# Kernel tuning notes

Hardware: AMD Instinct MI355X
Metric: run time of the kernel (lower is better)

## Reference

```python
import jax, jax.numpy as jnp
import numpy as np

CTX = 1024   # context_window
D = 512      # emb_dim
B = 8        # batch


def make_rotary_matrix(ctx, d):
    """Dense block-diagonal RoPE rotation matrices R: [ctx, d, d]."""
    pos = jnp.arange(ctx, dtype=jnp.float32)[:, None]          # [ctx, 1]
    i = jnp.arange(d // 2, dtype=jnp.float32)                  # [d/2]
    theta = pos / (10000.0 ** (2.0 * i / d))                   # [ctx, d/2]
    cos, sin = jnp.cos(theta), jnp.sin(theta)
    idx = jnp.arange(d // 2)
    R = jnp.zeros((ctx, d, d), jnp.float32)
    R = R.at[:, 2 * idx, 2 * idx].set(cos)
    R = R.at[:, 2 * idx, 2 * idx + 1].set(-sin)
    R = R.at[:, 2 * idx + 1, 2 * idx].set(sin)
    R = R.at[:, 2 * idx + 1, 2 * idx + 1].set(cos)
    return R


def setup_inputs() -> dict:
    key = jax.random.key(0)
    ks = jax.random.split(key, 8)
    s = 1.0 / np.sqrt(D)
    inp = {
        "x": jax.random.normal(ks[0], (B, CTX, D), jnp.float32),
        "w_q": jax.random.uniform(ks[1], (D, D), jnp.float32, -s, s),
        "b_q": jax.random.uniform(ks[2], (D,), jnp.float32, -s, s),
        "w_k": jax.random.uniform(ks[3], (D, D), jnp.float32, -s, s),
        "b_k": jax.random.uniform(ks[4], (D,), jnp.float32, -s, s),
        "w_v": jax.random.uniform(ks[5], (D, D), jnp.float32, -s, s),
        "b_v": jax.random.uniform(ks[6], (D,), jnp.float32, -s, s),
        "R": make_rotary_matrix(CTX, D),
        "kv_cache": 0,  # bool flag; does not affect output
    }
    return inp


def reference(x, w_q, b_q, w_k, b_k, w_v, b_v, R, kv_cache):
    B_, C, Dm = x.shape
    q = x @ w_q.T + b_q                      # [B, C, D]
    k = x @ w_k.T + b_k
    v = x @ w_v.T + b_v
    Rc = R[:C]                               # [C, D, D]
    # torch.bmm(q.transpose(0,1), R.transpose(1,2)).transpose(0,1)
    # out[b,c,e] = sum_d q[b,c,d] * R[c,e,d]
    q_rot = jnp.einsum("bcd,ced->bce", q, Rc)
    k_rot = jnp.einsum("bcd,ced->bce", k, Rc)
    # causal SDPA (eval mode: dropout omitted)
    scale = 1.0 / jnp.sqrt(jnp.asarray(Dm, jnp.float32))
    scores = jnp.einsum("bqe,bke->bqk", q_rot, k_rot) * scale   # [B, C, C]
    causal = jnp.tril(jnp.ones((C, C), bool))
    scores = jnp.where(causal, scores, jnp.finfo(scores.dtype).min)
    attn = jax.nn.softmax(scores, axis=-1)
    return jnp.einsum("bqk,bkd->bqd", attn, v)
```

## Files before the change

### kernel.cpp

```cpp
#include <hip/hip_runtime.h>

#define BATCH 8
#define CTXN  1024
#define DMODEL 512

using short8  = __attribute__((ext_vector_type(8))) short;
using f32x16  = __attribute__((ext_vector_type(16))) float;

typedef const void __attribute__((address_space(1)))* as1_cvp;
typedef void __attribute__((address_space(3)))* as3_vp;

__device__ __forceinline__ unsigned short f2bf(float f) {
  unsigned int u = __float_as_uint(f);
  u += 0x7fffu + ((u >> 16) & 1u);
  return (unsigned short)(u >> 16);
}
__device__ __forceinline__ float bf2f(unsigned short u) {
  return __uint_as_float((unsigned int)u << 16);
}

#define X4  1048576
#define W4  65536
#define CAST_BLOCKS 4864
__global__ __launch_bounds__(256) void prep_all(const float* __restrict__ x,
                                                const float* __restrict__ wq,
                                                const float* __restrict__ wk,
                                                const float* __restrict__ wv,
                                                unsigned short* __restrict__ xb,
                                                unsigned short* __restrict__ wb,
                                                float2* __restrict__ tab) {
  if (blockIdx.x < CAST_BLOCKS) {
    int gid = blockIdx.x * 256 + threadIdx.x;
    const float4* src; ushort4* dst;
    if (gid < X4)                { src = (const float4*)x  + gid;              dst = (ushort4*)xb + gid; }
    else if (gid < X4 + W4)      { int o = gid - X4;        src = (const float4*)wq + o; dst = (ushort4*)wb + o; }
    else if (gid < X4 + 2 * W4)  { int o = gid - X4 - W4;   src = (const float4*)wk + o; dst = (ushort4*)(wb + 262144) + o; }
    else                         { int o = gid - X4 - 2*W4; src = (const float4*)wv + o; dst = (ushort4*)(wb + 524288) + o; }
    float4 f = *src;
    ushort4 u;
    u.x = f2bf(f.x); u.y = f2bf(f.y); u.z = f2bf(f.z); u.w = f2bf(f.w);
    *dst = u;
  } else {
    int c = blockIdx.x - CAST_BLOCKS;
    int i = threadIdx.x;
    float freq = exp2f((float)i * (-13.287712379549449f / 256.0f));
    float th = (float)c * freq;
    float sn, cs;
    sincosf(th, &sn, &cs);
    tab[c * 256 + i] = make_float2(cs, sn);
  }
}


__device__ __forceinline__ void issue_tile(const unsigned short* __restrict__ gA, int ldA,
                                           const unsigned short* __restrict__ gB, int ldB,
                                           unsigned short* sA, unsigned short* sB,
                                           int slot, int tid) {
  unsigned short* dA = sA + (slot << 13);
  unsigned short* dB = sB + (slot << 13);
#pragma unroll
  for (int c = 0; c < 4; ++c) {
    int li  = (c << 8) + tid;
    int row = li >> 3;
    int ch  = (li & 7) ^ (row & 7);
    __builtin_amdgcn_global_load_lds((as1_cvp)(gA + (size_t)row * ldA + (ch << 3)),
                                     (as3_vp)(dA + (li << 3)), 16, 0, 0);
  }
#pragma unroll
  for (int c = 0; c < 4; ++c) {
    int li  = (c << 8) + tid;
    int row = li >> 3;
    int ch  = (li & 7) ^ (row & 7);
    __builtin_amdgcn_global_load_lds((as1_cvp)(gB + (size_t)row * ldB + (ch << 3)),
                                     (as3_vp)(dB + (li << 3)), 16, 0, 0);
  }
}

__device__ __forceinline__ void gemm_pipe(const unsigned short* __restrict__ gA, int ldA,
                                          const unsigned short* __restrict__ gB, int ldB,
                                          int nt, unsigned short* sA, unsigned short* sB,
                                          int tid, f32x16 acc[2][2]) {
  const int l = tid & 63, w = tid >> 6, wr = w >> 1, wc = w & 1;
  const int cl = l & 31, hi = l >> 5;
  int aoff[2][4], boff[2][4];
#pragma unroll
  for (int m = 0; m < 2; ++m) {
    int ra = wr * 64 + m * 32 + cl;
    int rb = wc * 64 + m * 32 + cl;
#pragma unroll
    for (int ks = 0; ks < 4; ++ks) {
      int kc = ks * 2 + hi;
      aoff[m][ks] = ra * 64 + ((kc ^ (ra & 7)) << 3);
      boff[m][ks] = rb * 64 + ((kc ^ (rb & 7)) << 3);
    }
  }
  issue_tile(gA, ldA, gB, ldB, sA, sB, 0, tid);
  issue_tile(gA + 64, ldA, gB + 64, ldB, sA, sB, 1, tid);
  asm volatile("s_waitcnt vmcnt(8)" ::: "memory");
  __builtin_amdgcn_s_barrier();
  __builtin_amdgcn_sched_barrier(0);

  for (int t = 0; t < nt; ++t) {
    const unsigned short* sAb = sA + ((t & 1) << 13);
    const unsigned short* sBb = sB + ((t & 1) << 13);
    short8 af[2][4], bfv[2][4];
    af[0][0] = *(const short8*)(sAb + aoff[0][0]);
    af[1][0] = *(const short8*)(sAb + aoff[1][0]);
    bfv[0][0] = *(const short8*)(sBb + boff[0][0]);
    bfv[1][0] = *(const short8*)(sBb + boff[1][0]);
#pragma unroll
    for (int ks = 0; ks < 3; ++ks) {
      af[0][ks + 1] = *(const short8*)(sAb + aoff[0][ks + 1]);
      af[1][ks + 1] = *(const short8*)(sAb + aoff[1][ks + 1]);
      bfv[0][ks + 1] = *(const short8*)(sBb + boff[0][ks + 1]);
      bfv[1][ks + 1] = *(const short8*)(sBb + boff[1][ks + 1]);
      asm volatile("s_waitcnt lgkmcnt(4)" ::: "memory");
      __builtin_amdgcn_sched_barrier(0);
      __builtin_amdgcn_s_setprio(1);
#pragma unroll
      for (int m = 0; m < 2; ++m)
#pragma unroll
        for (int n = 0; n < 2; ++n)
          acc[m][n] = __builtin_amdgcn_mfma_f32_32x32x16_bf16(af[m][ks], bfv[n][ks], acc[m][n], 0, 0, 0);
      __builtin_amdgcn_s_setprio(0);
    }
    asm volatile("s_waitcnt lgkmcnt(0)" ::: "memory");
    __builtin_amdgcn_sched_barrier(0);
    __builtin_amdgcn_s_barrier();
    if (t + 2 < nt) {
      issue_tile(gA + (size_t)(t + 2) * 64, ldA, gB + (size_t)(t + 2) * 64, ldB, sA, sB, t & 1, tid);
      asm volatile("s_waitcnt vmcnt(8)" ::: "memory");
    } else {
      asm volatile("s_waitcnt vmcnt(0)" ::: "memory");
    }
    __builtin_amdgcn_sched_barrier(0);
    __builtin_amdgcn_s_setprio(1);
#pragma unroll
    for (int m = 0; m < 2; ++m)
#pragma unroll
      for (int n = 0; n < 2; ++n)
        acc[m][n] = __builtin_amdgcn_mfma_f32_32x32x16_bf16(af[m][3], bfv[n][3], acc[m][n], 0, 0, 0);
    __builtin_amdgcn_s_setprio(0);
    __builtin_amdgcn_s_barrier();
    __builtin_amdgcn_sched_barrier(0);
  }
}


__global__ __launch_bounds__(256) void qkv_kernel(const unsigned short* __restrict__ xb,
                                                  const unsigned short* __restrict__ wb,
                                                  const float* __restrict__ bq,
                                                  const float* __restrict__ bk,
                                                  const float* __restrict__ bv,
                                                  const float2* __restrict__ tab,
                                                  unsigned short* __restrict__ qrot,
                                                  unsigned short* __restrict__ krot,
                                                  unsigned short* __restrict__ vt) {
  __shared__ __align__(16) unsigned short sA[2 * 8192];
  __shared__ __align__(16) unsigned short sB[2 * 8192];
  int t = threadIdx.x, w = t >> 6, l = t & 63, wr = w >> 1, wc = w & 1;
  int cl = l & 31, hi = l >> 5;
  int m0 = blockIdx.x * 128, n0 = blockIdx.y * 128;
  f32x16 acc[2][2] = {};
  gemm_pipe(xb + (size_t)m0 * 512, 512, wb + (size_t)n0 * 512, 512, 8, sA, sB, t, acc);

  int sec = n0 >> 9;
  const float* bias = (sec == 0) ? bq : (sec == 1) ? bk : bv;
  unsigned short* qk_dst = (sec == 0) ? qrot : krot;
#pragma unroll
  for (int n = 0; n < 2; ++n) {
    int eg = n0 + wc * 64 + n * 32 + cl;
    int e  = eg & 511;
    float bsv = bias[e];
    if (sec < 2) {
      int i2 = e >> 1;
#pragma unroll
      for (int m = 0; m < 2; ++m) {
        int rowb = m0 + wr * 64 + m * 32 + 4 * hi;
#pragma unroll
        for (int r = 0; r < 16; ++r) {
          int mg = rowb + (r & 3) + 8 * (r >> 2);
          int cpos = mg & (CTXN - 1);
          float val  = acc[m][n][r] + bsv;
          float part = __shfl_xor(val, 1);
          float2 cs  = tab[cpos * 256 + i2];
          float o = (e & 1) ? fmaf(part, cs.y, val * cs.x)
                            : fmaf(-part, cs.y, val * cs.x);
          qk_dst[(size_t)mg * 512 + e] = f2bf(o);
        }
      }
    } else {
#pragma unroll
      for (int m = 0; m < 2; ++m) {
        int rowb0 = m0 + wr * 64 + m * 32 + 4 * hi;
#pragma unroll
        for (int q = 0; q < 4; ++q) {
          int rowb = rowb0 + 8 * q;
          int bidx = rowb >> 10;
          int cpos = rowb & (CTXN - 1);
          ushort4 pk;
          pk.x = f2bf(acc[m][n][q * 4 + 0] + bsv);
          pk.y = f2bf(acc[m][n][q * 4 + 1] + bsv);
          pk.z = f2bf(acc[m][n][q * 4 + 2] + bsv);
          pk.w = f2bf(acc[m][n][q * 4 + 3] + bsv);
          *(ushort4*)(vt + ((size_t)bidx * 512 + e) * 1024 + cpos) = pk;
        }
      }
    }
  }
}

__device__ const unsigned char TRI_IT[36] = {0,1,1,2,2,2,3,3,3,3,4,4,4,4,4,5,5,5,5,5,5,
                                             6,6,6,6,6,6,6,7,7,7,7,7,7,7,7};
__device__ const unsigned char TRI_JT[36] = {0,0,1,0,1,2,0,1,2,3,0,1,2,3,4,0,1,2,3,4,5,
                                             0,1,2,3,4,5,6,0,1,2,3,4,5,6,7};

__global__ __launch_bounds__(256) void scores_kernel(const unsigned short* __restrict__ qr,
                                                     const unsigned short* __restrict__ kr,
                                                     unsigned short* __restrict__ S) {
  int it = TRI_IT[blockIdx.x], jt = TRI_JT[blockIdx.x], b = blockIdx.y;
  __shared__ __align__(16) unsigned short sA[2 * 8192];
  __shared__ __align__(16) unsigned short sB[2 * 8192];
  int t = threadIdx.x, w = t >> 6, l = t & 63, wr = w >> 1, wc = w & 1;
  int cl = l & 31, hi = l >> 5;
  const unsigned short* A  = qr + ((size_t)b << 19) + (size_t)it * 128 * 512;
  const unsigned short* Bp = kr + ((size_t)b << 19) + (size_t)jt * 128 * 512;
  f32x16 acc[2][2] = {};
  gemm_pipe(A, 512, Bp, 512, 8, sA, sB, t, acc);

  const float scale = 0.04419417382415922f;
  unsigned short* Sb = S + ((size_t)b << 20);
#pragma unroll
  for (int m = 0; m < 2; ++m) {
    int iqb = it * 128 + wr * 64 + m * 32 + 4 * hi;
#pragma unroll
    for (int n = 0; n < 2; ++n) {
      int j = jt * 128 + wc * 64 + n * 32 + cl;
#pragma unroll
      for (int r = 0; r < 16; ++r)
        Sb[(size_t)(iqb + (r & 3) + 8 * (r >> 2)) * 1024 + j] = f2bf(acc[m][n][r] * scale);
    }
  }
}

__global__ __launch_bounds__(256) void softmax_kernel(const unsigned short* __restrict__ S,
                                                      unsigned short* __restrict__ P) {
  int w = threadIdx.x >> 6, l = threadIdx.x & 63;
  int i = blockIdx.x * 4 + w;
  int b = blockIdx.y;
  const unsigned short* row = S + ((size_t)b << 20) + (size_t)i * 1024;
  unsigned short* prow = P + ((size_t)b << 20) + (size_t)i * 1024;
  int len  = i + 1;
  int jmax = ((i >> 7) + 1) << 7;
  float v[16];
  float mx = -3.4e38f;
#pragma unroll
  for (int c = 0; c < 2; ++c) {
    short8 raw = *(const short8*)(row + c * 512 + l * 8);
#pragma unroll
    for (int jj = 0; jj < 8; ++jj) {
      int j = c * 512 + l * 8 + jj;
      float f = bf2f((unsigned short)raw[jj]);
      v[c * 8 + jj] = (j < len) ? f : -3.4e38f;
      mx = fmaxf(mx, v[c * 8 + jj]);
    }
  }
#pragma unroll
  for (int o = 32; o > 0; o >>= 1) mx = fmaxf(mx, __shfl_xor(mx, o));
  float sm = 0.0f;
#pragma unroll
  for (int p = 0; p < 16; ++p) {
    int j = (p >> 3) * 512 + l * 8 + (p & 7);
    v[p] = (j < len) ? __expf(v[p] - mx) : 0.0f;
    sm += v[p];
  }
#pragma unroll
  for (int o = 32; o > 0; o >>= 1) sm += __shfl_xor(sm, o);
  float inv = 1.0f / sm;
#pragma unroll
  for (int c = 0; c < 2; ++c) {
    int jbase = c * 512 + l * 8;
    if (jbase < jmax) {
      short8 outv;
#pragma unroll
      for (int jj = 0; jj < 8; ++jj) outv[jj] = (short)f2bf(v[c * 8 + jj] * inv);
      *(short8*)(prow + jbase) = outv;
    }
  }
}

__global__ __launch_bounds__(256) void pv_kernel(const unsigned short* __restrict__ P,
                                                 const unsigned short* __restrict__ vt,
                                                 float* __restrict__ out) {
  int it = blockIdx.x, nt2 = blockIdx.y, b = blockIdx.z;
  __shared__ __align__(16) unsigned short sA[2 * 8192];
  __shared__ __align__(16) unsigned short sB[2 * 8192];
  int t = threadIdx.x, w = t >> 6, l = t & 63, wr = w >> 1, wc = w & 1;
  int cl = l & 31, hi = l >> 5;
  const unsigned short* A  = P  + ((size_t)b << 20) + (size_t)it * 128 * 1024;
  const unsigned short* Bp = vt + ((size_t)b << 19) + (size_t)nt2 * 128 * 1024;
  int nt = (it + 1) * 2;
  f32x16 acc[2][2] = {};
  gemm_pipe(A, 1024, Bp, 1024, nt, sA, sB, t, acc);

  float* ob = out + ((size_t)b << 19);
#pragma unroll
  for (int m = 0; m < 2; ++m) {
    int iqb = it * 128 + wr * 64 + m * 32 + 4 * hi;
#pragma unroll
    for (int n = 0; n < 2; ++n) {
      int d = nt2 * 128 + wc * 64 + n * 32 + cl;
#pragma unroll
      for (int r = 0; r < 16; ++r)
        ob[(size_t)(iqb + (r & 3) + 8 * (r >> 2)) * 512 + d] = acc[m][n][r];
    }
  }
}

extern "C" void kernel_launch(void* const* d_in, const int* in_sizes, int n_in,
                              void* d_out, int out_size, void* d_ws, size_t ws_size,
                              hipStream_t stream) {
  const float* x  = (const float*)d_in[0];
  const float* wq = (const float*)d_in[1];
  const float* bq = (const float*)d_in[2];
  const float* wk = (const float*)d_in[3];
  const float* bk = (const float*)d_in[4];
  const float* wv = (const float*)d_in[5];
  const float* bv = (const float*)d_in[6];
  float* out = (float*)d_out;

  char* ws = (char*)d_ws;
  float2*         tab  = (float2*)(ws);
  unsigned short* xb   = (unsigned short*)(ws + (2ull  << 20));
  unsigned short* wb   = (unsigned short*)(ws + (10ull << 20));
  unsigned short* qrot = (unsigned short*)(ws + (12ull << 20));
  unsigned short* krot = (unsigned short*)(ws + (20ull << 20));
  unsigned short* vt   = (unsigned short*)(ws + (28ull << 20));
  unsigned short* S    = (unsigned short*)(ws + (36ull << 20));
  unsigned short* P    = (unsigned short*)(ws + (52ull << 20));

  prep_all<<<dim3(CAST_BLOCKS + CTXN), dim3(256), 0, stream>>>(x, wq, wk, wv, xb, wb, tab);
  qkv_kernel<<<dim3(64, 12), dim3(256), 0, stream>>>(xb, wb, bq, bk, bv, tab, qrot, krot, vt);
  scores_kernel<<<dim3(36, BATCH), dim3(256), 0, stream>>>(qrot, krot, S);
  softmax_kernel<<<dim3(256, BATCH), dim3(256), 0, stream>>>(S, P);
  pv_kernel<<<dim3(8, 4, BATCH), dim3(256), 0, stream>>>(P, vt, out);
}
```

Before: 77.79 us.

## Use 8 waves per block with 2x4 wave grid in shared GEMM pipeline

Each 128x128 GEMM tile is now computed by 512 threads (8 waves in a 2x4 layout) instead of 256 (4 waves in 2x2), so each wave owns a 64x32 sub-tile with two accumulators. Loads per thread into LDS are halved and the waitcnt thresholds are adjusted to match. The aim is more waves per CU to hide latency and a lower register footprint per wave. In exchange, each wave gets less B-fragment reuse and barrier cost rises with more waves per block.

```diff
diff --git a/kernel.cpp b/kernel.cpp
--- a/kernel.cpp
+++ b/kernel.cpp
@@ -59,16 +59,16 @@
   unsigned short* dA = sA + (slot << 13);
   unsigned short* dB = sB + (slot << 13);
 #pragma unroll
-  for (int c = 0; c < 4; ++c) {
-    int li  = (c << 8) + tid;
+  for (int c = 0; c < 2; ++c) {
+    int li  = (c << 9) + tid;
     int row = li >> 3;
     int ch  = (li & 7) ^ (row & 7);
     __builtin_amdgcn_global_load_lds((as1_cvp)(gA + (size_t)row * ldA + (ch << 3)),
                                      (as3_vp)(dA + (li << 3)), 16, 0, 0);
   }
 #pragma unroll
-  for (int c = 0; c < 4; ++c) {
-    int li  = (c << 8) + tid;
+  for (int c = 0; c < 2; ++c) {
+    int li  = (c << 9) + tid;
     int row = li >> 3;
     int ch  = (li & 7) ^ (row & 7);
     __builtin_amdgcn_global_load_lds((as1_cvp)(gB + (size_t)row * ldB + (ch << 3)),
@@ -79,49 +79,50 @@
 __device__ __forceinline__ void gemm_pipe(const unsigned short* __restrict__ gA, int ldA,
                                           const unsigned short* __restrict__ gB, int ldB,
                                           int nt, unsigned short* sA, unsigned short* sB,
-                                          int tid, f32x16 acc[2][2]) {
-  const int l = tid & 63, w = tid >> 6, wr = w >> 1, wc = w & 1;
+                                          int tid, f32x16 acc[2]) {
+  const int l = tid & 63, w = tid >> 6, wr = w >> 2, wc = w & 3;
   const int cl = l & 31, hi = l >> 5;
-  int aoff[2][4], boff[2][4];
+  int aoff[2][4], boff[4];
 #pragma unroll
   for (int m = 0; m < 2; ++m) {
     int ra = wr * 64 + m * 32 + cl;
-    int rb = wc * 64 + m * 32 + cl;
 #pragma unroll
     for (int ks = 0; ks < 4; ++ks) {
       int kc = ks * 2 + hi;
       aoff[m][ks] = ra * 64 + ((kc ^ (ra & 7)) << 3);
-      boff[m][ks] = rb * 64 + ((kc ^ (rb & 7)) << 3);
+    }
+  }
+  {
+    int rb = wc * 32 + cl;
+#pragma unroll
+    for (int ks = 0; ks < 4; ++ks) {
+      int kc = ks * 2 + hi;
+      boff[ks] = rb * 64 + ((kc ^ (rb & 7)) << 3);
     }
   }
   issue_tile(gA, ldA, gB, ldB, sA, sB, 0, tid);
   issue_tile(gA + 64, ldA, gB + 64, ldB, sA, sB, 1, tid);
-  asm volatile("s_waitcnt vmcnt(8)" ::: "memory");
+  asm volatile("s_waitcnt vmcnt(4)" ::: "memory");
   __builtin_amdgcn_s_barrier();
   __builtin_amdgcn_sched_barrier(0);
 
   for (int t = 0; t < nt; ++t) {
     const unsigned short* sAb = sA + ((t & 1) << 13);
     const unsigned short* sBb = sB + ((t & 1) << 13);
-    short8 af[2][4], bfv[2][4];
+    short8 af[2][4], bfv[4];
     af[0][0] = *(const short8*)(sAb + aoff[0][0]);
     af[1][0] = *(const short8*)(sAb + aoff[1][0]);
-    bfv[0][0] = *(const short8*)(sBb + boff[0][0]);
-    bfv[1][0] = *(const short8*)(sBb + boff[1][0]);
+    bfv[0]   = *(const short8*)(sBb + boff[0]);
 #pragma unroll
     for (int ks = 0; ks < 3; ++ks) {
       af[0][ks + 1] = *(const short8*)(sAb + aoff[0][ks + 1]);
       af[1][ks + 1] = *(const short8*)(sAb + aoff[1][ks + 1]);
-      bfv[0][ks + 1] = *(const short8*)(sBb + boff[0][ks + 1]);
-      bfv[1][ks + 1] = *(const short8*)(sBb + boff[1][ks + 1]);
-      asm volatile("s_waitcnt lgkmcnt(4)" ::: "memory");
+      bfv[ks + 1]   = *(const short8*)(sBb + boff[ks + 1]);
+      asm volatile("s_waitcnt lgkmcnt(3)" ::: "memory");
       __builtin_amdgcn_sched_barrier(0);
       __builtin_amdgcn_s_setprio(1);
-#pragma unroll
-      for (int m = 0; m < 2; ++m)
-#pragma unroll
-        for (int n = 0; n < 2; ++n)
-          acc[m][n] = __builtin_amdgcn_mfma_f32_32x32x16_bf16(af[m][ks], bfv[n][ks], acc[m][n], 0, 0, 0);
+      acc[0] = __builtin_amdgcn_mfma_f32_32x32x16_bf16(af[0][ks], bfv[ks], acc[0], 0, 0, 0);
+      acc[1] = __builtin_amdgcn_mfma_f32_32x32x16_bf16(af[1][ks], bfv[ks], acc[1], 0, 0, 0);
       __builtin_amdgcn_s_setprio(0);
     }
     asm volatile("s_waitcnt lgkmcnt(0)" ::: "memory");
@@ -129,17 +130,14 @@
     __builtin_amdgcn_s_barrier();
     if (t + 2 < nt) {
       issue_tile(gA + (size_t)(t + 2) * 64, ldA, gB + (size_t)(t + 2) * 64, ldB, sA, sB, t & 1, tid);
-      asm volatile("s_waitcnt vmcnt(8)" ::: "memory");
+      asm volatile("s_waitcnt vmcnt(4)" ::: "memory");
     } else {
       asm volatile("s_waitcnt vmcnt(0)" ::: "memory");
     }
     __builtin_amdgcn_sched_barrier(0);
     __builtin_amdgcn_s_setprio(1);
-#pragma unroll
-    for (int m = 0; m < 2; ++m)
-#pragma unroll
-      for (int n = 0; n < 2; ++n)
-        acc[m][n] = __builtin_amdgcn_mfma_f32_32x32x16_bf16(af[m][3], bfv[n][3], acc[m][n], 0, 0, 0);
+    acc[0] = __builtin_amdgcn_mfma_f32_32x32x16_bf16(af[0][3], bfv[3], acc[0], 0, 0, 0);
+    acc[1] = __builtin_amdgcn_mfma_f32_32x32x16_bf16(af[1][3], bfv[3], acc[1], 0, 0, 0);
     __builtin_amdgcn_s_setprio(0);
     __builtin_amdgcn_s_barrier();
     __builtin_amdgcn_sched_barrier(0);
@@ -147,64 +145,60 @@
 }
 
 
-__global__ __launch_bounds__(256) void qkv_kernel(const unsigned short* __restrict__ xb,
-                                                  const unsigned short* __restrict__ wb,
-                                                  const float* __restrict__ bq,
-                                                  const float* __restrict__ bk,
-                                                  const float* __restrict__ bv,
-                                                  const float2* __restrict__ tab,
-                                                  unsigned short* __restrict__ qrot,
-                                                  unsigned short* __restrict__ krot,
-                                                  unsigned short* __restrict__ vt) {
+__global__ __launch_bounds__(512, 4) void qkv_kernel(const unsigned short* __restrict__ xb,
+                                                     const unsigned short* __restrict__ wb,
+                                                     const float* __restrict__ bq,
+                                                     const float* __restrict__ bk,
+                                                     const float* __restrict__ bv,
+                                                     const float2* __restrict__ tab,
+                                                     unsigned short* __restrict__ qrot,
+                                                     unsigned short* __restrict__ krot,
+                                                     unsigned short* __restrict__ vt) {
   __shared__ __align__(16) unsigned short sA[2 * 8192];
   __shared__ __align__(16) unsigned short sB[2 * 8192];
-  int t = threadIdx.x, w = t >> 6, l = t & 63, wr = w >> 1, wc = w & 1;
+  int t = threadIdx.x, w = t >> 6, l = t & 63, wr = w >> 2, wc = w & 3;
   int cl = l & 31, hi = l >> 5;
   int m0 = blockIdx.x * 128, n0 = blockIdx.y * 128;
-  f32x16 acc[2][2] = {};
+  f32x16 acc[2] = {};
   gemm_pipe(xb + (size_t)m0 * 512, 512, wb + (size_t)n0 * 512, 512, 8, sA, sB, t, acc);
 
   int sec = n0 >> 9;
   const float* bias = (sec == 0) ? bq : (sec == 1) ? bk : bv;
   unsigned short* qk_dst = (sec == 0) ? qrot : krot;
-#pragma unroll
-  for (int n = 0; n < 2; ++n) {
-    int eg = n0 + wc * 64 + n * 32 + cl;
-    int e  = eg & 511;
-    float bsv = bias[e];
-    if (sec < 2) {
-      int i2 = e >> 1;
-#pragma unroll
-      for (int m = 0; m < 2; ++m) {
-        int rowb = m0 + wr * 64 + m * 32 + 4 * hi;
-#pragma unroll
-        for (int r = 0; r < 16; ++r) {
-          int mg = rowb + (r & 3) + 8 * (r >> 2);
-          int cpos = mg & (CTXN - 1);
-          float val  = acc[m][n][r] + bsv;
-          float part = __shfl_xor(val, 1);
-          float2 cs  = tab[cpos * 256 + i2];
-          float o = (e & 1) ? fmaf(part, cs.y, val * cs.x)
-                            : fmaf(-part, cs.y, val * cs.x);
-          qk_dst[(size_t)mg * 512 + e] = f2bf(o);
-        }
+  int e = (n0 + wc * 32 + cl) & 511;
+  float bsv = bias[e];
+  if (sec < 2) {
+    int i2 = e >> 1;
+#pragma unroll
+    for (int m = 0; m < 2; ++m) {
+      int rowb = m0 + wr * 64 + m * 32 + 4 * hi;
+#pragma unroll
+      for (int r = 0; r < 16; ++r) {
+        int mg = rowb + (r & 3) + 8 * (r >> 2);
+        int cpos = mg & (CTXN - 1);
+        float val  = acc[m][r] + bsv;
+        float part = __shfl_xor(val, 1);
+        float2 cs  = tab[cpos * 256 + i2];
+        float o = (e & 1) ? fmaf(part, cs.y, val * cs.x)
+                          : fmaf(-part, cs.y, val * cs.x);
+        qk_dst[(size_t)mg * 512 + e] = f2bf(o);
       }
-    } else {
-#pragma unroll
-      for (int m = 0; m < 2; ++m) {
-        int rowb0 = m0 + wr * 64 + m * 32 + 4 * hi;
-#pragma unroll
-        for (int q = 0; q < 4; ++q) {
-          int rowb = rowb0 + 8 * q;
-          int bidx = rowb >> 10;
-          int cpos = rowb & (CTXN - 1);
-          ushort4 pk;
-          pk.x = f2bf(acc[m][n][q * 4 + 0] + bsv);
-          pk.y = f2bf(acc[m][n][q * 4 + 1] + bsv);
-          pk.z = f2bf(acc[m][n][q * 4 + 2] + bsv);
-          pk.w = f2bf(acc[m][n][q * 4 + 3] + bsv);
-          *(ushort4*)(vt + ((size_t)bidx * 512 + e) * 1024 + cpos) = pk;
-        }
+    }
+  } else {
+#pragma unroll
+    for (int m = 0; m < 2; ++m) {
+      int rowb0 = m0 + wr * 64 + m * 32 + 4 * hi;
+#pragma unroll
+      for (int q = 0; q < 4; ++q) {
+        int rowb = rowb0 + 8 * q;
+        int bidx = rowb >> 10;
+        int cpos = rowb & (CTXN - 1);
+        ushort4 pk;
+        pk.x = f2bf(acc[m][q * 4 + 0] + bsv);
+        pk.y = f2bf(acc[m][q * 4 + 1] + bsv);
+        pk.z = f2bf(acc[m][q * 4 + 2] + bsv);
+        pk.w = f2bf(acc[m][q * 4 + 3] + bsv);
+        *(ushort4*)(vt + ((size_t)bidx * 512 + e) * 1024 + cpos) = pk;
       }
     }
   }
@@ -215,31 +209,28 @@
 __device__ const unsigned char TRI_JT[36] = {0,0,1,0,1,2,0,1,2,3,0,1,2,3,4,0,1,2,3,4,5,
                                              0,1,2,3,4,5,6,0,1,2,3,4,5,6,7};
 
-__global__ __launch_bounds__(256) void scores_kernel(const unsigned short* __restrict__ qr,
-                                                     const unsigned short* __restrict__ kr,
-                                                     unsigned short* __restrict__ S) {
+__global__ __launch_bounds__(512, 4) void scores_kernel(const unsigned short* __restrict__ qr,
+                                                        const unsigned short* __restrict__ kr,
+                                                        unsigned short* __restrict__ S) {
   int it = TRI_IT[blockIdx.x], jt = TRI_JT[blockIdx.x], b = blockIdx.y;
   __shared__ __align__(16) unsigned short sA[2 * 8192];
   __shared__ __align__(16) unsigned short sB[2 * 8192];
-  int t = threadIdx.x, w = t >> 6, l = t & 63, wr = w >> 1, wc = w & 1;
+  int t = threadIdx.x, w = t >> 6, l = t & 63, wr = w >> 2, wc = w & 3;
   int cl = l & 31, hi = l >> 5;
   const unsigned short* A  = qr + ((size_t)b << 19) + (size_t)it * 128 * 512;
   const unsigned short* Bp = kr + ((size_t)b << 19) + (size_t)jt * 128 * 512;
-  f32x16 acc[2][2] = {};
+  f32x16 acc[2] = {};
   gemm_pipe(A, 512, Bp, 512, 8, sA, sB, t, acc);
 
   const float scale = 0.04419417382415922f;
   unsigned short* Sb = S + ((size_t)b << 20);
+  int j = jt * 128 + wc * 32 + cl;
 #pragma unroll
   for (int m = 0; m < 2; ++m) {
     int iqb = it * 128 + wr * 64 + m * 32 + 4 * hi;
 #pragma unroll
-    for (int n = 0; n < 2; ++n) {
-      int j = jt * 128 + wc * 64 + n * 32 + cl;
-#pragma unroll
-      for (int r = 0; r < 16; ++r)
-        Sb[(size_t)(iqb + (r & 3) + 8 * (r >> 2)) * 1024 + j] = f2bf(acc[m][n][r] * scale);
-    }
+    for (int r = 0; r < 16; ++r)
+      Sb[(size_t)(iqb + (r & 3) + 8 * (r >> 2)) * 1024 + j] = f2bf(acc[m][r] * scale);
   }
 }
 
@@ -289,31 +280,28 @@
   }
 }
 
-__global__ __launch_bounds__(256) void pv_kernel(const unsigned short* __restrict__ P,
-                                                 const unsigned short* __restrict__ vt,
-                                                 float* __restrict__ out) {
+__global__ __launch_bounds__(512, 4) void pv_kernel(const unsigned short* __restrict__ P,
+                                                    const unsigned short* __restrict__ vt,
+                                                    float* __restrict__ out) {
   int it = blockIdx.x, nt2 = blockIdx.y, b = blockIdx.z;
   __shared__ __align__(16) unsigned short sA[2 * 8192];
   __shared__ __align__(16) unsigned short sB[2 * 8192];
-  int t = threadIdx.x, w = t >> 6, l = t & 63, wr = w >> 1, wc = w & 1;
+  int t = threadIdx.x, w = t >> 6, l = t & 63, wr = w >> 2, wc = w & 3;
   int cl = l & 31, hi = l >> 5;
   const unsigned short* A  = P  + ((size_t)b << 20) + (size_t)it * 128 * 1024;
   const unsigned short* Bp = vt + ((size_t)b << 19) + (size_t)nt2 * 128 * 1024;
   int nt = (it + 1) * 2;
-  f32x16 acc[2][2] = {};
+  f32x16 acc[2] = {};
   gemm_pipe(A, 1024, Bp, 1024, nt, sA, sB, t, acc);
 
   float* ob = out + ((size_t)b << 19);
+  int d = nt2 * 128 + wc * 32 + cl;
 #pragma unroll
   for (int m = 0; m < 2; ++m) {
     int iqb = it * 128 + wr * 64 + m * 32 + 4 * hi;
 #pragma unroll
-    for (int n = 0; n < 2; ++n) {
-      int d = nt2 * 128 + wc * 64 + n * 32 + cl;
-#pragma unroll
-      for (int r = 0; r < 16; ++r)
-        ob[(size_t)(iqb + (r & 3) + 8 * (r >> 2)) * 512 + d] = acc[m][n][r];
-    }
+    for (int r = 0; r < 16; ++r)
+      ob[(size_t)(iqb + (r & 3) + 8 * (r >> 2)) * 512 + d] = acc[m][r];
   }
 }
 
@@ -340,8 +328,8 @@
   unsigned short* P    = (unsigned short*)(ws + (52ull << 20));
 
   prep_all<<<dim3(CAST_BLOCKS + CTXN), dim3(256), 0, stream>>>(x, wq, wk, wv, xb, wb, tab);
-  qkv_kernel<<<dim3(64, 12), dim3(256), 0, stream>>>(xb, wb, bq, bk, bv, tab, qrot, krot, vt);
-  scores_kernel<<<dim3(36, BATCH), dim3(256), 0, stream>>>(qrot, krot, S);
+  qkv_kernel<<<dim3(64, 12), dim3(512), 0, stream>>>(xb, wb, bq, bk, bv, tab, qrot, krot, vt);
+  scores_kernel<<<dim3(36, BATCH), dim3(512), 0, stream>>>(qrot, krot, S);
   softmax_kernel<<<dim3(256, BATCH), dim3(256), 0, stream>>>(S, P);
-  pv_kernel<<<dim3(8, 4, BATCH), dim3(256), 0, stream>>>(P, vt, out);
-}
+  pv_kernel<<<dim3(8, 4, BATCH), dim3(512), 0, stream>>>(P, vt, out);
+}
```

After: 77.15 us. Within noise of the previous version (-0.8%).
